# Performance work log

Measured on AMD Instinct MI355X. Metric: run time of the kernel, lower is better.

The kernel has to match this reference:

```python
import jax, jax.numpy as jnp
import numpy as np

EMBED = 512
NH = 8
HD = EMBED // NH
NL = 12
FFN = 2048
TD = 16  # latent_channels * patch_size**2 = 4*4


def _ln(x, g, b):
    m = x.mean(-1, keepdims=True)
    v = ((x - m) ** 2).mean(-1, keepdims=True)
    return (x - m) * jax.lax.rsqrt(v + 1e-5) * g + b


def _pos_emb(H, W, d):
    # faithful to get_2d_rope_embedding: cosine 1D embeddings along h and w, concatenated
    dh = d // 2
    inv = 1.0 / (10000.0 ** (jnp.arange(dh, dtype=jnp.float32) / dh))
    peh = jnp.cos(jnp.arange(H, dtype=jnp.float32)[:, None] * inv[None, :])  # (H, dh)
    pew = jnp.cos(jnp.arange(W, dtype=jnp.float32)[:, None] * inv[None, :])  # (W, dh)
    pe = jnp.concatenate([
        jnp.broadcast_to(peh[:, None, :], (H, W, dh)),
        jnp.broadcast_to(pew[None, :, :], (H, W, dh)),
    ], axis=-1)
    return pe.reshape(H * W, d)


def setup_inputs() -> dict:
    key = jax.random.key(0)
    ks = jax.random.split(key, 20)
    B, L = 8, 1024
    s = 0.02
    inp = {
        'x': jax.random.normal(ks[0], (B, L, TD), jnp.float32),
        'token_mask': jnp.ones((B, L), jnp.int32),
        'W_in': s * jax.random.normal(ks[1], (TD, EMBED), jnp.float32),
        'b_in': jnp.zeros((EMBED,), jnp.float32),
        'ln1_g': jnp.ones((NL, EMBED), jnp.float32),
        'ln1_b': jnp.zeros((NL, EMBED), jnp.float32),
        'Wq': s * jax.random.normal(ks[2], (NL, EMBED, EMBED), jnp.float32),
        'Wk': s * jax.random.normal(ks[3], (NL, EMBED, EMBED), jnp.float32),
        'Wv': s * jax.random.normal(ks[4], (NL, EMBED, EMBED), jnp.float32),
        'Wo': s * jax.random.normal(ks[5], (NL, EMBED, EMBED), jnp.float32),
        'ln2_g': jnp.ones((NL, EMBED), jnp.float32),
        'ln2_b': jnp.zeros((NL, EMBED), jnp.float32),
        'W1': s * jax.random.normal(ks[6], (NL, EMBED, FFN), jnp.float32),
        'W2': s * jax.random.normal(ks[7], (NL, EMBED, FFN), jnp.float32),
        'W3': s * jax.random.normal(ks[8], (NL, FFN, EMBED), jnp.float32),
        'W_out': s * jax.random.normal(ks[9], (EMBED, TD), jnp.float32),
        'b_out': jnp.zeros((TD,), jnp.float32),
        'H': 32,
        'W': 32,
    }
    return inp


def reference(x, token_mask, W_in, b_in, ln1_g, ln1_b, Wq, Wk, Wv, Wo,
              ln2_g, ln2_b, W1, W2, W3, W_out, b_out, H, W):
    B, L, _ = x.shape
    scale = 1.0 / np.sqrt(HD).astype(np.float32)
    h = x @ W_in + b_in + _pos_emb(H, W, EMBED)[None]  # (B, L, E)
    # (B,1,1,L) additive mask, -1e9 at padded positions
    mask = (token_mask == 0)[:, None, None, :].astype(h.dtype) * (-1e9)

    def block(h, p):
        g1, b1, wq, wk, wv, wo, g2, b2, w1, w2, w3 = p
        xn = _ln(h, g1, b1)
        q = (xn @ wq).reshape(B, L, NH, HD)
        k = (xn @ wk).reshape(B, L, NH, HD)
        v = (xn @ wv).reshape(B, L, NH, HD)
        s = jnp.einsum('blhd,bmhd->bhlm', q, k) * scale + mask
        a = jax.nn.softmax(s, axis=-1)
        o = jnp.einsum('bhlm,bmhd->blhd', a, v).reshape(B, L, EMBED) @ wo
        h = h + o
        xn = _ln(h, g2, b2)
        h = h + (jax.nn.silu(xn @ w1) * (xn @ w2)) @ w3
        return h, None

    h, _ = jax.lax.scan(block, h, (ln1_g, ln1_b, Wq, Wk, Wv, Wo, ln2_g, ln2_b, W1, W2, W3))
    return h @ W_out + b_out  # (B, L, TD)
```

## Files before the change

kernel.cpp:

```cpp
#include <hip/hip_runtime.h>

typedef __attribute__((ext_vector_type(8))) short short8;
typedef __attribute__((ext_vector_type(4))) float f32x4;
typedef __attribute__((ext_vector_type(4))) unsigned short us4;

#define MFMA_BF16(a,b,c) __builtin_amdgcn_mfma_f32_16x16x32_bf16((a),(b),(c),0,0,0)

__device__ __forceinline__ unsigned short f2bf(float f) {
  unsigned int u = __float_as_uint(f);
  u += 0x7fffu + ((u >> 16) & 1u);
  return (unsigned short)(u >> 16);
}

__global__ __launch_bounds__(256) void wtrans_kernel(const float* __restrict__ src,
                                                     unsigned short* __restrict__ dst,
                                                     int R, int C) {
  __shared__ float tile[32][33];
  int c0 = blockIdx.x * 32, r0 = blockIdx.y * 32;
  const float* s = src + (size_t)blockIdx.z * R * C;
  unsigned short* d = dst + (size_t)blockIdx.z * R * C;
  int tx = threadIdx.x, ty = threadIdx.y;
#pragma unroll
  for (int i = 0; i < 32; i += 8)
    tile[ty + i][tx] = s[(size_t)(r0 + ty + i) * C + c0 + tx];
  __syncthreads();
#pragma unroll
  for (int i = 0; i < 32; i += 8)
    d[(size_t)(c0 + ty + i) * R + r0 + tx] = f2bf(tile[tx][ty + i]);
}

__global__ __launch_bounds__(128) void embed_kernel(const float* __restrict__ x,
                                                    const float* __restrict__ Win,
                                                    const float* __restrict__ bin,
                                                    float* __restrict__ h) {
  __shared__ float xs[16];
  int m = blockIdx.x, t = threadIdx.x;
  if (t < 16) xs[t] = x[m * 16 + t];
  __syncthreads();
  int l = m & 1023, hi = l >> 5, wi = l & 31;
#pragma unroll
  for (int e0 = 0; e0 < 512; e0 += 128) {
    int e = e0 + t;
    float a = bin[e];
#pragma unroll
    for (int kk = 0; kk < 16; kk++) a += xs[kk] * Win[kk * 512 + e];
    int j = e & 255;
    float p = (e < 256) ? (float)hi : (float)wi;
    float inv = expf((float)j * (-9.210340371976184f / 256.0f));
    a += cosf(p * inv);
    h[(size_t)m * 512 + e] = a;
  }
}

__global__ __launch_bounds__(128) void ln_kernel(const float* __restrict__ h,
                                                 const float* __restrict__ gw,
                                                 const float* __restrict__ bw,
                                                 unsigned short* __restrict__ xn) {
  int m = blockIdx.x, t = threadIdx.x;
  f32x4 v = *(const f32x4*)&h[(size_t)m * 512 + t * 4];
  float s = v[0] + v[1] + v[2] + v[3];
  float q = v[0]*v[0] + v[1]*v[1] + v[2]*v[2] + v[3]*v[3];
#pragma unroll
  for (int o = 1; o < 64; o <<= 1) { s += __shfl_xor(s, o); q += __shfl_xor(q, o); }
  __shared__ float red[4];
  if ((t & 63) == 0) { red[(t >> 6) * 2] = s; red[(t >> 6) * 2 + 1] = q; }
  __syncthreads();
  s = red[0] + red[2]; q = red[1] + red[3];
  float mean = s * (1.0f / 512.0f);
  float var = q * (1.0f / 512.0f) - mean * mean;
  float rstd = rsqrtf(var + 1e-5f);
  f32x4 gg = *(const f32x4*)&gw[t * 4];
  f32x4 bb = *(const f32x4*)&bw[t * 4];
  us4 w;
#pragma unroll
  for (int r = 0; r < 4; r++) w[r] = f2bf((v[r] - mean) * rstd * gg[r] + bb[r]);
  *(us4*)&xn[(size_t)m * 512 + t * 4] = w;
}

__global__ __launch_bounds__(256) void qkv_gemm(const unsigned short* __restrict__ xn,
                                                const unsigned short* __restrict__ wtq,
                                                const unsigned short* __restrict__ wtk,
                                                const unsigned short* __restrict__ wtv,
                                                unsigned short* __restrict__ qo,
                                                unsigned short* __restrict__ ko,
                                                unsigned short* __restrict__ vo) {
  __shared__ short8 As[512];
  __shared__ short8 Bs[512];
  int n0 = blockIdx.x * 128, m0 = blockIdx.y * 128;
  int sel = n0 >> 9;
  const short8* wt = (const short8*)(sel == 0 ? wtq : sel == 1 ? wtk : wtv);
  unsigned short* out = sel == 0 ? qo : sel == 1 ? ko : vo;
  int nw = n0 & 511;
  const short8* A8 = (const short8*)xn;
  int tid = threadIdx.x, wid = tid >> 6, lane = tid & 63;
  int wr = wid >> 1, wc = wid & 1, c16 = lane & 15, g = lane >> 4;
  int subA = wid * 2;
  f32x4 acc[4][4] = {};
  short8 ra[2], rb[2];
#pragma unroll
  for (int s = 0; s < 2; s++) {
    ra[s] = A8[(size_t)(m0 + (subA + s) * 16 + c16) * 64 + g];
    rb[s] = wt[(size_t)(nw + (subA + s) * 16 + c16) * 64 + g];
  }
  for (int kt = 0; kt < 16; kt++) {
    __syncthreads();
#pragma unroll
    for (int s = 0; s < 2; s++) {
      As[(subA + s) * 64 + lane] = ra[s];
      Bs[(subA + s) * 64 + lane] = rb[s];
    }
    if (kt < 15) {
#pragma unroll
      for (int s = 0; s < 2; s++) {
        ra[s] = A8[(size_t)(m0 + (subA + s) * 16 + c16) * 64 + (kt + 1) * 4 + g];
        rb[s] = wt[(size_t)(nw + (subA + s) * 16 + c16) * 64 + (kt + 1) * 4 + g];
      }
    }
    __syncthreads();
    short8 af[4], bf[4];
#pragma unroll
    for (int mf = 0; mf < 4; mf++) af[mf] = As[(wr * 4 + mf) * 64 + lane];
#pragma unroll
    for (int nf = 0; nf < 4; nf++) bf[nf] = Bs[(wc * 4 + nf) * 64 + lane];
#pragma unroll
    for (int mf = 0; mf < 4; mf++)
#pragma unroll
      for (int nf = 0; nf < 4; nf++)
        acc[mf][nf] = MFMA_BF16(af[mf], bf[nf], acc[mf][nf]);
  }
#pragma unroll
  for (int mf = 0; mf < 4; mf++)
#pragma unroll
    for (int nf = 0; nf < 4; nf++) {
      int col = nw + wc * 64 + nf * 16 + c16;
#pragma unroll
      for (int r = 0; r < 4; r++) {
        int row = m0 + wr * 64 + mf * 16 + g * 4 + r;
        out[(size_t)row * 512 + col] = f2bf(acc[mf][nf][r]);
      }
    }
}

__global__ __launch_bounds__(256) void gemm_res(const unsigned short* __restrict__ A,
                                                const unsigned short* __restrict__ Wt,
                                                float* __restrict__ h, int Kd8, int nkt) {
  __shared__ short8 As[512];
  __shared__ short8 Bs[512];
  int n0 = blockIdx.x * 128, m0 = blockIdx.y * 128;
  const short8* A8 = (const short8*)A;
  const short8* W8 = (const short8*)Wt;
  int tid = threadIdx.x, wid = tid >> 6, lane = tid & 63;
  int wr = wid >> 1, wc = wid & 1, c16 = lane & 15, g = lane >> 4;
  int subA = wid * 2;
  f32x4 acc[4][4] = {};
  short8 ra[2], rb[2];
#pragma unroll
  for (int s = 0; s < 2; s++) {
    ra[s] = A8[(size_t)(m0 + (subA + s) * 16 + c16) * Kd8 + g];
    rb[s] = W8[(size_t)(n0 + (subA + s) * 16 + c16) * Kd8 + g];
  }
  for (int kt = 0; kt < nkt; kt++) {
    __syncthreads();
#pragma unroll
    for (int s = 0; s < 2; s++) {
      As[(subA + s) * 64 + lane] = ra[s];
      Bs[(subA + s) * 64 + lane] = rb[s];
    }
    if (kt + 1 < nkt) {
#pragma unroll
      for (int s = 0; s < 2; s++) {
        ra[s] = A8[(size_t)(m0 + (subA + s) * 16 + c16) * Kd8 + (kt + 1) * 4 + g];
        rb[s] = W8[(size_t)(n0 + (subA + s) * 16 + c16) * Kd8 + (kt + 1) * 4 + g];
      }
    }
    __syncthreads();
    short8 af[4], bf[4];
#pragma unroll
    for (int mf = 0; mf < 4; mf++) af[mf] = As[(wr * 4 + mf) * 64 + lane];
#pragma unroll
    for (int nf = 0; nf < 4; nf++) bf[nf] = Bs[(wc * 4 + nf) * 64 + lane];
#pragma unroll
    for (int mf = 0; mf < 4; mf++)
#pragma unroll
      for (int nf = 0; nf < 4; nf++)
        acc[mf][nf] = MFMA_BF16(af[mf], bf[nf], acc[mf][nf]);
  }
#pragma unroll
  for (int mf = 0; mf < 4; mf++)
#pragma unroll
    for (int nf = 0; nf < 4; nf++) {
      int col = n0 + wc * 64 + nf * 16 + c16;
#pragma unroll
      for (int r = 0; r < 4; r++) {
        int row = m0 + wr * 64 + mf * 16 + g * 4 + r;
        h[(size_t)row * 512 + col] += acc[mf][nf][r];
      }
    }
}

__global__ __launch_bounds__(256) void ffn_gemm(const unsigned short* __restrict__ xn,
                                                const unsigned short* __restrict__ w1t,
                                                const unsigned short* __restrict__ w2t,
                                                unsigned short* __restrict__ gout) {
  __shared__ short8 As[512];
  __shared__ short8 B1s[512];
  __shared__ short8 B2s[512];
  int n0 = blockIdx.x * 128, m0 = blockIdx.y * 128;
  const short8* A8 = (const short8*)xn;
  const short8* W18 = (const short8*)w1t;
  const short8* W28 = (const short8*)w2t;
  int tid = threadIdx.x, wid = tid >> 6, lane = tid & 63;
  int wr = wid >> 1, wc = wid & 1, c16 = lane & 15, g = lane >> 4;
  int subA = wid * 2;
  f32x4 acc1[4][4] = {};
  f32x4 acc2[4][4] = {};
  short8 ra[2], rb1[2], rb2[2];
#pragma unroll
  for (int s = 0; s < 2; s++) {
    ra[s]  = A8 [(size_t)(m0 + (subA + s) * 16 + c16) * 64 + g];
    rb1[s] = W18[(size_t)(n0 + (subA + s) * 16 + c16) * 64 + g];
    rb2[s] = W28[(size_t)(n0 + (subA + s) * 16 + c16) * 64 + g];
  }
  for (int kt = 0; kt < 16; kt++) {
    __syncthreads();
#pragma unroll
    for (int s = 0; s < 2; s++) {
      As [(subA + s) * 64 + lane] = ra[s];
      B1s[(subA + s) * 64 + lane] = rb1[s];
      B2s[(subA + s) * 64 + lane] = rb2[s];
    }
    if (kt < 15) {
#pragma unroll
      for (int s = 0; s < 2; s++) {
        ra[s]  = A8 [(size_t)(m0 + (subA + s) * 16 + c16) * 64 + (kt + 1) * 4 + g];
        rb1[s] = W18[(size_t)(n0 + (subA + s) * 16 + c16) * 64 + (kt + 1) * 4 + g];
        rb2[s] = W28[(size_t)(n0 + (subA + s) * 16 + c16) * 64 + (kt + 1) * 4 + g];
      }
    }
    __syncthreads();
    short8 af[4], b1f[4], b2f[4];
#pragma unroll
    for (int mf = 0; mf < 4; mf++) af[mf] = As[(wr * 4 + mf) * 64 + lane];
#pragma unroll
    for (int nf = 0; nf < 4; nf++) {
      b1f[nf] = B1s[(wc * 4 + nf) * 64 + lane];
      b2f[nf] = B2s[(wc * 4 + nf) * 64 + lane];
    }
#pragma unroll
    for (int mf = 0; mf < 4; mf++)
#pragma unroll
      for (int nf = 0; nf < 4; nf++) {
        acc1[mf][nf] = MFMA_BF16(af[mf], b1f[nf], acc1[mf][nf]);
        acc2[mf][nf] = MFMA_BF16(af[mf], b2f[nf], acc2[mf][nf]);
      }
  }
#pragma unroll
  for (int mf = 0; mf < 4; mf++)
#pragma unroll
    for (int nf = 0; nf < 4; nf++) {
      int col = n0 + wc * 64 + nf * 16 + c16;
#pragma unroll
      for (int r = 0; r < 4; r++) {
        int row = m0 + wr * 64 + mf * 16 + g * 4 + r;
        float xx = acc1[mf][nf][r];
        float yy = acc2[mf][nf][r];
        float sg = xx / (1.0f + __expf(-xx));
        gout[(size_t)row * 2048 + col] = f2bf(sg * yy);
      }
    }
}

__global__ __launch_bounds__(256) void vtrans_kernel(const unsigned short* __restrict__ v,
                                                     unsigned short* __restrict__ vt) {
  __shared__ __align__(16) unsigned short tile[64][72];
  int bid = blockIdx.x;
  int bh = bid >> 4, lt = bid & 15;
  int b = bh >> 3, hh = bh & 7;
  int t = threadIdx.x;
  int lr = t >> 2, d0 = (t & 3) * 16;
  const unsigned short* src = v + (size_t)(b * 1024 + lt * 64 + lr) * 512 + hh * 64 + d0;
  *(short8*)&tile[lr][d0] = *(const short8*)src;
  *(short8*)&tile[lr][d0 + 8] = *(const short8*)(src + 8);
  __syncthreads();
  int d = t & 63, l0 = (t >> 6) * 16;
  unsigned short* dst = vt + (size_t)(bh * 64 + d) * 1024 + lt * 64 + l0;
  short8 w0, w1;
#pragma unroll
  for (int i = 0; i < 8; i++) w0[i] = (short)tile[l0 + i][d];
#pragma unroll
  for (int i = 0; i < 8; i++) w1[i] = (short)tile[l0 + 8 + i][d];
  *(short8*)dst = w0;
  *(short8*)(dst + 8) = w1;
}

__global__ __launch_bounds__(256) void attn_kernel(const unsigned short* __restrict__ q,
                                                   const unsigned short* __restrict__ k,
                                                   const unsigned short* __restrict__ vt,
                                                   const int* __restrict__ tmsk,
                                                   unsigned short* __restrict__ o) {
  __shared__ short8 Ks[512];
  __shared__ short8 Vs[512];
  __shared__ uint2  Pb[2048];
  __shared__ f32x4  maskv[256];

  int bid = blockIdx.x;
  int qb = bid & 7;
  int bh = bid >> 3;
  int b = bh >> 3, hh = bh & 7;
  int tid = threadIdx.x, wid = tid >> 6, lane = tid & 63;
  int c16 = lane & 15, gq = lane >> 4;
  int qrow0 = qb * 128 + wid * 32;

  const short8* q8 = (const short8*)q;
  const short8* k8 = (const short8*)k;
  const short8* v8 = (const short8*)vt;

  short8 qf[2][2];
#pragma unroll
  for (int nf = 0; nf < 2; nf++)
#pragma unroll
    for (int dc = 0; dc < 2; dc++)
      qf[nf][dc] = q8[(size_t)(b * 1024 + qrow0 + nf * 16 + c16) * 64 + hh * 8 + dc * 4 + gq];

  {
    int4 mm = ((const int4*)(tmsk + b * 1024))[tid];
    f32x4 ma;
    ma[0] = (mm.x == 0) ? -1e9f : 0.0f;
    ma[1] = (mm.y == 0) ? -1e9f : 0.0f;
    ma[2] = (mm.z == 0) ? -1e9f : 0.0f;
    ma[3] = (mm.w == 0) ? -1e9f : 0.0f;
    maskv[tid] = ma;
  }

  short8 rk[2], rv[2];
#pragma unroll
  for (int s = 0; s < 2; s++) {
    int sub = wid * 2 + s;
    rk[s] = k8[(size_t)(b * 1024 + (sub >> 1) * 16 + c16) * 64 + hh * 8 + (sub & 1) * 4 + gq];
    rv[s] = v8[(size_t)(bh * 64 + (sub >> 1) * 16 + c16) * 128 + (sub & 1) * 4 + gq];
  }

  float mrun[2] = {-1e30f, -1e30f};
  float lrun[2] = {0.0f, 0.0f};
  f32x4 accO[4][2] = {};

  for (int kt = 0; kt < 16; kt++) {
    __syncthreads();
#pragma unroll
    for (int s = 0; s < 2; s++) {
      int sub = wid * 2 + s;
      Ks[sub * 64 + lane] = rk[s];
      Vs[sub * 64 + lane] = rv[s];
    }
    if (kt < 15) {
      int kt2 = kt + 1;
#pragma unroll
      for (int s = 0; s < 2; s++) {
        int sub = wid * 2 + s;
        rk[s] = k8[(size_t)(b * 1024 + kt2 * 64 + (sub >> 1) * 16 + c16) * 64 + hh * 8 + (sub & 1) * 4 + gq];
        rv[s] = v8[(size_t)(bh * 64 + (sub >> 1) * 16 + c16) * 128 + kt2 * 8 + (sub & 1) * 4 + gq];
      }
    }
    __syncthreads();

    f32x4 sT[4][2] = {};
#pragma unroll
    for (int mf = 0; mf < 4; mf++) {
      short8 ka0 = Ks[(mf * 2 + 0) * 64 + lane];
      short8 ka1 = Ks[(mf * 2 + 1) * 64 + lane];
#pragma unroll
      for (int nf = 0; nf < 2; nf++) {
        sT[mf][nf] = MFMA_BF16(ka0, qf[nf][0], sT[mf][nf]);
        sT[mf][nf] = MFMA_BF16(ka1, qf[nf][1], sT[mf][nf]);
      }
    }

#pragma unroll
    for (int nf = 0; nf < 2; nf++) {
      float pv[4][4];
      float tm = -1e30f;
#pragma unroll
      for (int mf = 0; mf < 4; mf++) {
        f32x4 mk = maskv[kt * 16 + mf * 4 + gq];
#pragma unroll
        for (int r = 0; r < 4; r++) {
          float sv = sT[mf][nf][r] * 0.125f + mk[r];
          pv[mf][r] = sv;
          tm = fmaxf(tm, sv);
        }
      }
      tm = fmaxf(tm, __shfl_xor(tm, 16));
      tm = fmaxf(tm, __shfl_xor(tm, 32));
      float mn = fmaxf(mrun[nf], tm);
      float fac = __expf(mrun[nf] - mn);
      mrun[nf] = mn;
      float ts = 0.0f;
#pragma unroll
      for (int mf = 0; mf < 4; mf++)
#pragma unroll
        for (int r = 0; r < 4; r++) {
          float p = __expf(pv[mf][r] - mn);
          pv[mf][r] = p;
          ts += p;
        }
      ts += __shfl_xor(ts, 16);
      ts += __shfl_xor(ts, 32);
      lrun[nf] = lrun[nf] * fac + ts;
#pragma unroll
      for (int dmf = 0; dmf < 4; dmf++) accO[dmf][nf] *= fac;
#pragma unroll
      for (int mf = 0; mf < 4; mf++) {
        unsigned lo = (unsigned)f2bf(pv[mf][0]) | ((unsigned)f2bf(pv[mf][1]) << 16);
        unsigned hi = (unsigned)f2bf(pv[mf][2]) | ((unsigned)f2bf(pv[mf][3]) << 16);
        int kk = mf >> 1;
        int gr = (mf & 1) * 2 + (gq >> 1);
        uint2 t2; t2.x = lo; t2.y = hi;
        Pb[wid * 512 + ((nf * 2 + kk) * 64 + gr * 16 + c16) * 2 + (gq & 1)] = t2;
      }
    }
    __syncthreads();

    const short8* Pb8 = (const short8*)Pb;
#pragma unroll
    for (int nf = 0; nf < 2; nf++) {
      short8 pb0 = Pb8[wid * 256 + (nf * 2 + 0) * 64 + lane];
      short8 pb1 = Pb8[wid * 256 + (nf * 2 + 1) * 64 + lane];
#pragma unroll
      for (int dmf = 0; dmf < 4; dmf++) {
        short8 va0 = Vs[(dmf * 2 + 0) * 64 + lane];
        short8 va1 = Vs[(dmf * 2 + 1) * 64 + lane];
        accO[dmf][nf] = MFMA_BF16(va0, pb0, accO[dmf][nf]);
        accO[dmf][nf] = MFMA_BF16(va1, pb1, accO[dmf][nf]);
      }
    }
  }

#pragma unroll
  for (int nf = 0; nf < 2; nf++) {
    float inv = 1.0f / lrun[nf];
    int row = b * 1024 + qrow0 + nf * 16 + c16;
#pragma unroll
    for (int dmf = 0; dmf < 4; dmf++) {
      us4 w;
#pragma unroll
      for (int r = 0; r < 4; r++) w[r] = f2bf(accO[dmf][nf][r] * inv);
      *(us4*)&o[(size_t)row * 512 + hh * 64 + dmf * 16 + gq * 4] = w;
    }
  }
}

__global__ __launch_bounds__(128) void out_kernel(const float* __restrict__ h,
                                                  const float* __restrict__ Wout,
                                                  const float* __restrict__ bout,
                                                  float* __restrict__ out) {
  __shared__ f32x4 hs4[8][128];
  __shared__ f32x4 Ws4[16][129];
  int t = threadIdx.x;
  int rb = blockIdx.x * 8;
  float* hsf = (float*)hs4;
  float* wsf = (float*)Ws4;
  for (int i = t; i < 4096; i += 128) hsf[i] = h[(size_t)rb * 512 + i];
  for (int i = t; i < 8192; i += 128) wsf[(i & 15) * 516 + (i >> 4)] = Wout[i];
  __syncthreads();
  int r = t >> 4, c = t & 15;
  float acc = bout[c];
  for (int k4 = 0; k4 < 128; k4++) {
    f32x4 a = hs4[r][k4];
    f32x4 w = Ws4[c][k4];
    acc += a[0]*w[0] + a[1]*w[1] + a[2]*w[2] + a[3]*w[3];
  }
  out[(rb + r) * 16 + c] = acc;
}

extern "C" void kernel_launch(void* const* d_in, const int* in_sizes, int n_in,
                              void* d_out, int out_size, void* d_ws, size_t ws_size,
                              hipStream_t stream) {
  const float* x    = (const float*)d_in[0];
  const int*   tmsk = (const int*)d_in[1];
  const float* Win  = (const float*)d_in[2];
  const float* bin  = (const float*)d_in[3];
  const float* ln1g = (const float*)d_in[4];
  const float* ln1b = (const float*)d_in[5];
  const float* Wq   = (const float*)d_in[6];
  const float* Wk   = (const float*)d_in[7];
  const float* Wv   = (const float*)d_in[8];
  const float* Wo   = (const float*)d_in[9];
  const float* ln2g = (const float*)d_in[10];
  const float* ln2b = (const float*)d_in[11];
  const float* W1   = (const float*)d_in[12];
  const float* W2   = (const float*)d_in[13];
  const float* W3   = (const float*)d_in[14];
  const float* Wout = (const float*)d_in[15];
  const float* bout = (const float*)d_in[16];
  float* outp = (float*)d_out;

  char* ws = (char*)d_ws;
  unsigned short* wtq = (unsigned short*)(ws + 0);
  unsigned short* wtk = (unsigned short*)(ws + 6291456);
  unsigned short* wtv = (unsigned short*)(ws + 12582912);
  unsigned short* wto = (unsigned short*)(ws + 18874368);
  unsigned short* wt1 = (unsigned short*)(ws + 25165824);
  unsigned short* wt2 = (unsigned short*)(ws + 50331648);
  unsigned short* wt3 = (unsigned short*)(ws + 75497472);
  float*          h   = (float*)(ws + 100663296);
  unsigned short* xn  = (unsigned short*)(ws + 117440512);
  unsigned short* qb  = (unsigned short*)(ws + 125829120);
  unsigned short* kb  = (unsigned short*)(ws + 134217728);
  unsigned short* vb  = (unsigned short*)(ws + 142606336);
  unsigned short* vtb = (unsigned short*)(ws + 150994944);
  unsigned short* ob  = (unsigned short*)(ws + 159383552);
  unsigned short* gb  = (unsigned short*)(ws + 167772160);

  dim3 tb(32, 8);
  wtrans_kernel<<<dim3(16, 16, 12), tb, 0, stream>>>(Wq, wtq, 512, 512);
  wtrans_kernel<<<dim3(16, 16, 12), tb, 0, stream>>>(Wk, wtk, 512, 512);
  wtrans_kernel<<<dim3(16, 16, 12), tb, 0, stream>>>(Wv, wtv, 512, 512);
  wtrans_kernel<<<dim3(16, 16, 12), tb, 0, stream>>>(Wo, wto, 512, 512);
  wtrans_kernel<<<dim3(64, 16, 12), tb, 0, stream>>>(W1, wt1, 512, 2048);
  wtrans_kernel<<<dim3(64, 16, 12), tb, 0, stream>>>(W2, wt2, 512, 2048);
  wtrans_kernel<<<dim3(16, 64, 12), tb, 0, stream>>>(W3, wt3, 2048, 512);

  embed_kernel<<<8192, 128, 0, stream>>>(x, Win, bin, h);

  for (int l = 0; l < 12; l++) {
    ln_kernel<<<8192, 128, 0, stream>>>(h, ln1g + l * 512, ln1b + l * 512, xn);
    qkv_gemm<<<dim3(12, 64), 256, 0, stream>>>(xn,
        wtq + (size_t)l * 262144, wtk + (size_t)l * 262144, wtv + (size_t)l * 262144,
        qb, kb, vb);
    vtrans_kernel<<<1024, 256, 0, stream>>>(vb, vtb);
    attn_kernel<<<512, 256, 0, stream>>>(qb, kb, vtb, tmsk, ob);
    gemm_res<<<dim3(4, 64), 256, 0, stream>>>(ob, wto + (size_t)l * 262144, h, 64, 16);
    ln_kernel<<<8192, 128, 0, stream>>>(h, ln2g + l * 512, ln2b + l * 512, xn);
    ffn_gemm<<<dim3(16, 64), 256, 0, stream>>>(xn,
        wt1 + (size_t)l * 1048576, wt2 + (size_t)l * 1048576, gb);
    gemm_res<<<dim3(4, 64), 256, 0, stream>>>(gb, wt3 + (size_t)l * 1048576, h, 256, 64);
  }
  out_kernel<<<1024, 128, 0, stream>>>(h, Wout, bout, outp);

  (void)in_sizes; (void)n_in; (void)out_size; (void)ws_size;
}
```

Baseline: 2.720 ms.

## Fuse V transpose into QKV GEMM, widen residual GEMM K-tile, swizzle attention blocks

The QKV GEMM now writes V directly in transposed (bh,d,l) layout, which removes the separate vtrans kernel and its global round trip. The residual GEMM stages a 64-wide K slice per iteration, halving the barrier count at the cost of twice the LDS. LayerNorm processes one row per wavefront with no shared-memory reduction, and attention blocks are remapped with an XCD-aware swizzle to improve L2 locality. The transposed V stores are 8-byte scattered writes, which may coalesce worse than before.

```diff
diff --git a/kernel.cpp b/kernel.cpp
--- a/kernel.cpp
+++ b/kernel.cpp
@@ -10,6 +10,10 @@
   unsigned int u = __float_as_uint(f);
   u += 0x7fffu + ((u >> 16) & 1u);
   return (unsigned short)(u >> 16);
+}
+
+__device__ __forceinline__ int xcd_swz(int lid, int nwg) {
+  return (lid & 7) * (nwg >> 3) + (lid >> 3);
 }
 
 __global__ __launch_bounds__(256) void wtrans_kernel(const float* __restrict__ src,
@@ -52,29 +56,32 @@
   }
 }
 
-__global__ __launch_bounds__(128) void ln_kernel(const float* __restrict__ h,
+__global__ __launch_bounds__(256) void ln_kernel(const float* __restrict__ h,
                                                  const float* __restrict__ gw,
                                                  const float* __restrict__ bw,
                                                  unsigned short* __restrict__ xn) {
-  int m = blockIdx.x, t = threadIdx.x;
-  f32x4 v = *(const f32x4*)&h[(size_t)m * 512 + t * 4];
-  float s = v[0] + v[1] + v[2] + v[3];
-  float q = v[0]*v[0] + v[1]*v[1] + v[2]*v[2] + v[3]*v[3];
+  int row = blockIdx.x * 4 + (threadIdx.x >> 6);
+  int lane = threadIdx.x & 63;
+  const f32x4* hr = (const f32x4*)&h[(size_t)row * 512];
+  f32x4 v0 = hr[lane], v1 = hr[lane + 64];
+  float s = v0[0]+v0[1]+v0[2]+v0[3] + v1[0]+v1[1]+v1[2]+v1[3];
+  float q = v0[0]*v0[0]+v0[1]*v0[1]+v0[2]*v0[2]+v0[3]*v0[3]
+          + v1[0]*v1[0]+v1[1]*v1[1]+v1[2]*v1[2]+v1[3]*v1[3];
 #pragma unroll
   for (int o = 1; o < 64; o <<= 1) { s += __shfl_xor(s, o); q += __shfl_xor(q, o); }
-  __shared__ float red[4];
-  if ((t & 63) == 0) { red[(t >> 6) * 2] = s; red[(t >> 6) * 2 + 1] = q; }
-  __syncthreads();
-  s = red[0] + red[2]; q = red[1] + red[3];
   float mean = s * (1.0f / 512.0f);
   float var = q * (1.0f / 512.0f) - mean * mean;
   float rstd = rsqrtf(var + 1e-5f);
-  f32x4 gg = *(const f32x4*)&gw[t * 4];
-  f32x4 bb = *(const f32x4*)&bw[t * 4];
-  us4 w;
-#pragma unroll
-  for (int r = 0; r < 4; r++) w[r] = f2bf((v[r] - mean) * rstd * gg[r] + bb[r]);
-  *(us4*)&xn[(size_t)m * 512 + t * 4] = w;
+  f32x4 g0 = ((const f32x4*)gw)[lane], g1 = ((const f32x4*)gw)[lane + 64];
+  f32x4 b0 = ((const f32x4*)bw)[lane], b1 = ((const f32x4*)bw)[lane + 64];
+  us4 w0, w1;
+#pragma unroll
+  for (int r = 0; r < 4; r++) {
+    w0[r] = f2bf((v0[r] - mean) * rstd * g0[r] + b0[r]);
+    w1[r] = f2bf((v1[r] - mean) * rstd * g1[r] + b1[r]);
+  }
+  *(us4*)&xn[(size_t)row * 512 + lane * 4] = w0;
+  *(us4*)&xn[(size_t)row * 512 + 256 + lane * 4] = w1;
 }
 
 __global__ __launch_bounds__(256) void qkv_gemm(const unsigned short* __restrict__ xn,
@@ -83,13 +90,12 @@
                                                 const unsigned short* __restrict__ wtv,
                                                 unsigned short* __restrict__ qo,
                                                 unsigned short* __restrict__ ko,
-                                                unsigned short* __restrict__ vo) {
+                                                unsigned short* __restrict__ vt) {
   __shared__ short8 As[512];
   __shared__ short8 Bs[512];
   int n0 = blockIdx.x * 128, m0 = blockIdx.y * 128;
   int sel = n0 >> 9;
   const short8* wt = (const short8*)(sel == 0 ? wtq : sel == 1 ? wtk : wtv);
-  unsigned short* out = sel == 0 ? qo : sel == 1 ? ko : vo;
   int nw = n0 & 511;
   const short8* A8 = (const short8*)xn;
   int tid = threadIdx.x, wid = tid >> 6, lane = tid & 63;
@@ -128,62 +134,86 @@
       for (int nf = 0; nf < 4; nf++)
         acc[mf][nf] = MFMA_BF16(af[mf], bf[nf], acc[mf][nf]);
   }
-#pragma unroll
-  for (int mf = 0; mf < 4; mf++)
-#pragma unroll
-    for (int nf = 0; nf < 4; nf++) {
-      int col = nw + wc * 64 + nf * 16 + c16;
-#pragma unroll
-      for (int r = 0; r < 4; r++) {
-        int row = m0 + wr * 64 + mf * 16 + g * 4 + r;
-        out[(size_t)row * 512 + col] = f2bf(acc[mf][nf][r]);
-      }
-    }
+  if (sel < 2) {
+    unsigned short* out = sel == 0 ? qo : ko;
+#pragma unroll
+    for (int mf = 0; mf < 4; mf++)
+#pragma unroll
+      for (int nf = 0; nf < 4; nf++) {
+        int col = nw + wc * 64 + nf * 16 + c16;
+#pragma unroll
+        for (int r = 0; r < 4; r++) {
+          int row = m0 + wr * 64 + mf * 16 + g * 4 + r;
+          out[(size_t)row * 512 + col] = f2bf(acc[mf][nf][r]);
+        }
+      }
+  } else {
+    int b8 = (m0 >> 10) * 8;
+    int loff = (m0 & 1023) + wr * 64;
+#pragma unroll
+    for (int mf = 0; mf < 4; mf++)
+#pragma unroll
+      for (int nf = 0; nf < 4; nf++) {
+        int c = nw + wc * 64 + nf * 16 + c16;
+        int bh = b8 + (c >> 6), d = c & 63;
+        us4 w;
+#pragma unroll
+        for (int r = 0; r < 4; r++) w[r] = f2bf(acc[mf][nf][r]);
+        *(us4*)&vt[(size_t)(bh * 64 + d) * 1024 + loff + mf * 16 + g * 4] = w;
+      }
+  }
 }
 
 __global__ __launch_bounds__(256) void gemm_res(const unsigned short* __restrict__ A,
                                                 const unsigned short* __restrict__ Wt,
-                                                float* __restrict__ h, int Kd8, int nkt) {
-  __shared__ short8 As[512];
-  __shared__ short8 Bs[512];
+                                                float* __restrict__ h, int Kd8, int nkt64) {
+  __shared__ short8 As[1024];
+  __shared__ short8 Bs[1024];
   int n0 = blockIdx.x * 128, m0 = blockIdx.y * 128;
   const short8* A8 = (const short8*)A;
   const short8* W8 = (const short8*)Wt;
   int tid = threadIdx.x, wid = tid >> 6, lane = tid & 63;
   int wr = wid >> 1, wc = wid & 1, c16 = lane & 15, g = lane >> 4;
-  int subA = wid * 2;
+  const short8* aSrc[4];
+  const short8* bSrc[4];
+#pragma unroll
+  for (int s = 0; s < 4; s++) {
+    int sub = wid * 4 + s, rg = sub >> 1, kc = sub & 1;
+    aSrc[s] = A8 + (size_t)(m0 + rg * 16 + c16) * Kd8 + kc * 4 + g;
+    bSrc[s] = W8 + (size_t)(n0 + rg * 16 + c16) * Kd8 + kc * 4 + g;
+  }
   f32x4 acc[4][4] = {};
-  short8 ra[2], rb[2];
-#pragma unroll
-  for (int s = 0; s < 2; s++) {
-    ra[s] = A8[(size_t)(m0 + (subA + s) * 16 + c16) * Kd8 + g];
-    rb[s] = W8[(size_t)(n0 + (subA + s) * 16 + c16) * Kd8 + g];
-  }
-  for (int kt = 0; kt < nkt; kt++) {
-    __syncthreads();
-#pragma unroll
-    for (int s = 0; s < 2; s++) {
-      As[(subA + s) * 64 + lane] = ra[s];
-      Bs[(subA + s) * 64 + lane] = rb[s];
-    }
-    if (kt + 1 < nkt) {
-#pragma unroll
-      for (int s = 0; s < 2; s++) {
-        ra[s] = A8[(size_t)(m0 + (subA + s) * 16 + c16) * Kd8 + (kt + 1) * 4 + g];
-        rb[s] = W8[(size_t)(n0 + (subA + s) * 16 + c16) * Kd8 + (kt + 1) * 4 + g];
-      }
-    }
-    __syncthreads();
-    short8 af[4], bf[4];
-#pragma unroll
-    for (int mf = 0; mf < 4; mf++) af[mf] = As[(wr * 4 + mf) * 64 + lane];
-#pragma unroll
-    for (int nf = 0; nf < 4; nf++) bf[nf] = Bs[(wc * 4 + nf) * 64 + lane];
-#pragma unroll
-    for (int mf = 0; mf < 4; mf++)
-#pragma unroll
-      for (int nf = 0; nf < 4; nf++)
-        acc[mf][nf] = MFMA_BF16(af[mf], bf[nf], acc[mf][nf]);
+  short8 ra[4], rb[4];
+#pragma unroll
+  for (int s = 0; s < 4; s++) { ra[s] = aSrc[s][0]; rb[s] = bSrc[s][0]; }
+  for (int kt = 0; kt < nkt64; kt++) {
+    __syncthreads();
+#pragma unroll
+    for (int s = 0; s < 4; s++) {
+      As[(wid * 4 + s) * 64 + lane] = ra[s];
+      Bs[(wid * 4 + s) * 64 + lane] = rb[s];
+    }
+    if (kt + 1 < nkt64) {
+#pragma unroll
+      for (int s = 0; s < 4; s++) {
+        ra[s] = aSrc[s][(kt + 1) * 8];
+        rb[s] = bSrc[s][(kt + 1) * 8];
+      }
+    }
+    __syncthreads();
+#pragma unroll
+    for (int kc = 0; kc < 2; kc++) {
+      short8 af[4], bf[4];
+#pragma unroll
+      for (int mf = 0; mf < 4; mf++) af[mf] = As[((wr * 4 + mf) * 2 + kc) * 64 + lane];
+#pragma unroll
+      for (int nf = 0; nf < 4; nf++) bf[nf] = Bs[((wc * 4 + nf) * 2 + kc) * 64 + lane];
+#pragma unroll
+      for (int mf = 0; mf < 4; mf++)
+#pragma unroll
+        for (int nf = 0; nf < 4; nf++)
+          acc[mf][nf] = MFMA_BF16(af[mf], bf[nf], acc[mf][nf]);
+    }
   }
 #pragma unroll
   for (int mf = 0; mf < 4; mf++)
@@ -270,29 +300,6 @@
     }
 }
 
-__global__ __launch_bounds__(256) void vtrans_kernel(const unsigned short* __restrict__ v,
-                                                     unsigned short* __restrict__ vt) {
-  __shared__ __align__(16) unsigned short tile[64][72];
-  int bid = blockIdx.x;
-  int bh = bid >> 4, lt = bid & 15;
-  int b = bh >> 3, hh = bh & 7;
-  int t = threadIdx.x;
-  int lr = t >> 2, d0 = (t & 3) * 16;
-  const unsigned short* src = v + (size_t)(b * 1024 + lt * 64 + lr) * 512 + hh * 64 + d0;
-  *(short8*)&tile[lr][d0] = *(const short8*)src;
-  *(short8*)&tile[lr][d0 + 8] = *(const short8*)(src + 8);
-  __syncthreads();
-  int d = t & 63, l0 = (t >> 6) * 16;
-  unsigned short* dst = vt + (size_t)(bh * 64 + d) * 1024 + lt * 64 + l0;
-  short8 w0, w1;
-#pragma unroll
-  for (int i = 0; i < 8; i++) w0[i] = (short)tile[l0 + i][d];
-#pragma unroll
-  for (int i = 0; i < 8; i++) w1[i] = (short)tile[l0 + 8 + i][d];
-  *(short8*)dst = w0;
-  *(short8*)(dst + 8) = w1;
-}
-
 __global__ __launch_bounds__(256) void attn_kernel(const unsigned short* __restrict__ q,
                                                    const unsigned short* __restrict__ k,
                                                    const unsigned short* __restrict__ vt,
@@ -303,9 +310,9 @@
   __shared__ uint2  Pb[2048];
   __shared__ f32x4  maskv[256];
 
-  int bid = blockIdx.x;
-  int qb = bid & 7;
-  int bh = bid >> 3;
+  int s = xcd_swz((int)blockIdx.x, 512);
+  int qb = s & 7;
+  int bh = s >> 3;
   int b = bh >> 3, hh = bh & 7;
   int tid = threadIdx.x, wid = tid >> 6, lane = tid & 63;
   int c16 = lane & 15, gq = lane >> 4;
@@ -334,10 +341,10 @@
 
   short8 rk[2], rv[2];
 #pragma unroll
-  for (int s = 0; s < 2; s++) {
-    int sub = wid * 2 + s;
-    rk[s] = k8[(size_t)(b * 1024 + (sub >> 1) * 16 + c16) * 64 + hh * 8 + (sub & 1) * 4 + gq];
-    rv[s] = v8[(size_t)(bh * 64 + (sub >> 1) * 16 + c16) * 128 + (sub & 1) * 4 + gq];
+  for (int ss = 0; ss < 2; ss++) {
+    int sub = wid * 2 + ss;
+    rk[ss] = k8[(size_t)(b * 1024 + (sub >> 1) * 16 + c16) * 64 + hh * 8 + (sub & 1) * 4 + gq];
+    rv[ss] = v8[(size_t)(bh * 64 + (sub >> 1) * 16 + c16) * 128 + (sub & 1) * 4 + gq];
   }
 
   float mrun[2] = {-1e30f, -1e30f};
@@ -347,18 +354,18 @@
   for (int kt = 0; kt < 16; kt++) {
     __syncthreads();
 #pragma unroll
-    for (int s = 0; s < 2; s++) {
-      int sub = wid * 2 + s;
-      Ks[sub * 64 + lane] = rk[s];
-      Vs[sub * 64 + lane] = rv[s];
+    for (int ss = 0; ss < 2; ss++) {
+      int sub = wid * 2 + ss;
+      Ks[sub * 64 + lane] = rk[ss];
+      Vs[sub * 64 + lane] = rv[ss];
     }
     if (kt < 15) {
       int kt2 = kt + 1;
 #pragma unroll
-      for (int s = 0; s < 2; s++) {
-        int sub = wid * 2 + s;
-        rk[s] = k8[(size_t)(b * 1024 + kt2 * 64 + (sub >> 1) * 16 + c16) * 64 + hh * 8 + (sub & 1) * 4 + gq];
-        rv[s] = v8[(size_t)(bh * 64 + (sub >> 1) * 16 + c16) * 128 + kt2 * 8 + (sub & 1) * 4 + gq];
+      for (int ss = 0; ss < 2; ss++) {
+        int sub = wid * 2 + ss;
+        rk[ss] = k8[(size_t)(b * 1024 + kt2 * 64 + (sub >> 1) * 16 + c16) * 64 + hh * 8 + (sub & 1) * 4 + gq];
+        rv[ss] = v8[(size_t)(bh * 64 + (sub >> 1) * 16 + c16) * 128 + kt2 * 8 + (sub & 1) * 4 + gq];
       }
     }
     __syncthreads();
@@ -506,7 +513,6 @@
   unsigned short* xn  = (unsigned short*)(ws + 117440512);
   unsigned short* qb  = (unsigned short*)(ws + 125829120);
   unsigned short* kb  = (unsigned short*)(ws + 134217728);
-  unsigned short* vb  = (unsigned short*)(ws + 142606336);
   unsigned short* vtb = (unsigned short*)(ws + 150994944);
   unsigned short* ob  = (unsigned short*)(ws + 159383552);
   unsigned short* gb  = (unsigned short*)(ws + 167772160);
@@ -523,17 +529,16 @@
   embed_kernel<<<8192, 128, 0, stream>>>(x, Win, bin, h);
 
   for (int l = 0; l < 12; l++) {
-    ln_kernel<<<8192, 128, 0, stream>>>(h, ln1g + l * 512, ln1b + l * 512, xn);
+    ln_kernel<<<2048, 256, 0, stream>>>(h, ln1g + l * 512, ln1b + l * 512, xn);
     qkv_gemm<<<dim3(12, 64), 256, 0, stream>>>(xn,
         wtq + (size_t)l * 262144, wtk + (size_t)l * 262144, wtv + (size_t)l * 262144,
-        qb, kb, vb);
-    vtrans_kernel<<<1024, 256, 0, stream>>>(vb, vtb);
+        qb, kb, vtb);
     attn_kernel<<<512, 256, 0, stream>>>(qb, kb, vtb, tmsk, ob);
-    gemm_res<<<dim3(4, 64), 256, 0, stream>>>(ob, wto + (size_t)l * 262144, h, 64, 16);
-    ln_kernel<<<8192, 128, 0, stream>>>(h, ln2g + l * 512, ln2b + l * 512, xn);
+    gemm_res<<<dim3(4, 64), 256, 0, stream>>>(ob, wto + (size_t)l * 262144, h, 64, 8);
+    ln_kernel<<<2048, 256, 0, stream>>>(h, ln2g + l * 512, ln2b + l * 512, xn);
     ffn_gemm<<<dim3(16, 64), 256, 0, stream>>>(xn,
         wt1 + (size_t)l * 1048576, wt2 + (size_t)l * 1048576, gb);
-    gemm_res<<<dim3(4, 64), 256, 0, stream>>>(gb, wt3 + (size_t)l * 1048576, h, 256, 64);
+    gemm_res<<<dim3(4, 64), 256, 0, stream>>>(gb, wt3 + (size_t)l * 1048576, h, 256, 32);
   }
   out_kernel<<<1024, 128, 0, stream>>>(h, Wout, bout, outp);
 
```

Measured after the change: 2.582 ms. 5.1% less time.
